# Kernel optimization log

Measured on AMD Instinct MI355X. Metric: run time of the kernel, lower is better.

## Reference

```python
import jax, jax.numpy as jnp
import numpy as np

N, H, E, A, T = 50000, 128, 800000, 16, 4


def setup_inputs() -> dict:
    key = jax.random.key(0)
    ks = jax.random.split(key, 12)
    s = 1.0 / np.sqrt(H + A)
    s2 = 1.0 / np.sqrt(H)
    return {
        "h": jax.random.normal(ks[0], (N, H), dtype=jnp.float32),
        "edge_index": jax.random.randint(ks[1], (2, E), 0, N, dtype=jnp.int32),
        "edge_type": jax.random.randint(ks[2], (E,), 0, T, dtype=jnp.int32),
        "edge_attr": jax.random.normal(ks[3], (E, A), dtype=jnp.float32),
        # per-edge-type 2-layer MLP params
        "W1": jax.random.uniform(ks[4], (T, H + A, H), minval=-s, maxval=s, dtype=jnp.float32),
        "b1": jax.random.uniform(ks[5], (T, H), minval=-s, maxval=s, dtype=jnp.float32),
        "W2": jax.random.uniform(ks[6], (T, H, H), minval=-s2, maxval=s2, dtype=jnp.float32),
        "b2": jax.random.uniform(ks[7], (T, H), minval=-s2, maxval=s2, dtype=jnp.float32),
        # GRUCell params (torch layout: [3H, H] with gate order r, z, n)
        "w_ih": jax.random.uniform(ks[8], (3 * H, H), minval=-s2, maxval=s2, dtype=jnp.float32),
        "w_hh": jax.random.uniform(ks[9], (3 * H, H), minval=-s2, maxval=s2, dtype=jnp.float32),
        "b_ih": jax.random.uniform(ks[10], (3 * H,), minval=-s2, maxval=s2, dtype=jnp.float32),
        "b_hh": jax.random.uniform(ks[11], (3 * H,), minval=-s2, maxval=s2, dtype=jnp.float32),
    }


def reference(h, edge_index, edge_type, edge_attr, W1, b1, W2, b2, w_ih, w_hh, b_ih, b_hh):
    src, dst = edge_index[0], edge_index[1]
    h_in = jnp.concatenate([h[src], edge_attr], axis=-1)  # [E, H+A]
    # per-edge-type MLP; loop over small fixed num_edge_types, mask-select
    m = jnp.zeros((h_in.shape[0], H), dtype=h.dtype)
    for t in range(T):
        mt = jax.nn.relu(h_in @ W1[t] + b1[t]) @ W2[t] + b2[t]  # [E, H]
        m = jnp.where((edge_type == t)[:, None], mt, m)
    # scatter-add messages to destination nodes
    msg = jax.ops.segment_sum(m, dst, num_segments=h.shape[0])  # [N, H]
    # GRUCell(msg, h) with torch gate order r, z, n
    gi = msg @ w_ih.T + b_ih  # [N, 3H]
    gh = h @ w_hh.T + b_hh
    i_r, i_z, i_n = jnp.split(gi, 3, axis=-1)
    h_r, h_z, h_n = jnp.split(gh, 3, axis=-1)
    r = jax.nn.sigmoid(i_r + h_r)
    z = jax.nn.sigmoid(i_z + h_z)
    n = jnp.tanh(i_n + r * h_n)
    return (1.0 - z) * n + z * h
```

## Files before the change

kernel.cpp:

```cpp
#include <hip/hip_runtime.h>
#include <stdint.h>

#define Hh 128
#define Aa 16
#define Tt 4
#define K1 144
#define K1P 160
#define W1T_LD 168
#define WG_LD  136

typedef float f32x4 __attribute__((ext_vector_type(4)));
typedef __bf16 bf16x8 __attribute__((ext_vector_type(8)));
typedef unsigned short u16x8 __attribute__((ext_vector_type(8)));
typedef unsigned short u16x4 __attribute__((ext_vector_type(4)));
typedef unsigned short u16x2 __attribute__((ext_vector_type(2)));

static __device__ __forceinline__ unsigned short f2bf(float f) {
    unsigned u = __builtin_bit_cast(unsigned, f);
    u += 0x7fffu + ((u >> 16) & 1u);
    return (unsigned short)(u >> 16);
}

static __device__ __forceinline__ float bf2f(unsigned short u) {
    return __builtin_bit_cast(float, (unsigned)u << 16);
}

static __device__ __forceinline__ bf16x8 pack8(const float* __restrict__ x) {
    f32x4 a = *(const f32x4*)x;
    f32x4 b = *(const f32x4*)(x + 4);
    u16x8 t;
    t[0] = f2bf(a[0]); t[1] = f2bf(a[1]); t[2] = f2bf(a[2]); t[3] = f2bf(a[3]);
    t[4] = f2bf(b[0]); t[5] = f2bf(b[1]); t[6] = f2bf(b[2]); t[7] = f2bf(b[3]);
    return __builtin_bit_cast(bf16x8, t);
}

static __device__ __forceinline__ bf16x8 zero_bf8() {
    u16x8 z = {0, 0, 0, 0, 0, 0, 0, 0};
    return __builtin_bit_cast(bf16x8, z);
}

__global__ void cast_all_kernel(
    const float* __restrict__ h, const float* __restrict__ wih, const float* __restrict__ whh,
    unsigned short* __restrict__ h_bf, unsigned short* __restrict__ wihb,
    unsigned short* __restrict__ whhb, int n0, int n1, int n2)
{
    int i = blockIdx.x * blockDim.x + threadIdx.x;
    if (i >= n2) return;
    const float* s; unsigned short* d; int off;
    if (i < n0)      { s = h;   d = h_bf; off = i; }
    else if (i < n1) { s = wih; d = wihb; off = i - n0; }
    else             { s = whh; d = whhb; off = i - n1; }
    f32x4 v = *(const f32x4*)(s + (size_t)off * 4);
    u16x4 o;
    o[0] = f2bf(v[0]); o[1] = f2bf(v[1]); o[2] = f2bf(v[2]); o[3] = f2bf(v[3]);
    *(u16x4*)(d + (size_t)off * 4) = o;
}

__global__ void w1t_kernel(const float* __restrict__ W1, unsigned short* __restrict__ W1Tbf) {
    __shared__ float tile[16][129];
    const int b = blockIdx.x;
    const int t = b / 10, kb = b % 10;
    const int k0 = kb * 16;
    const int tid = threadIdx.x;
    for (int e = tid; e < 16 * 128; e += 256) {
        int k = e >> 7, n = e & 127;
        tile[k][n] = (k0 + k < K1) ? W1[((size_t)t * K1 + k0 + k) * Hh + n] : 0.f;
    }
    __syncthreads();
    for (int e = tid; e < 128 * 16; e += 256) {
        int n = e >> 4, kk = e & 15;
        W1Tbf[((size_t)t * Hh + n) * K1P + k0 + kk] = f2bf(tile[kk][n]);
    }
}

__global__ void w2t_kernel(const float* __restrict__ W2, unsigned short* __restrict__ W2Tbf) {
    __shared__ float tile[16][129];
    const int b = blockIdx.x;
    const int t = b >> 3, kb = b & 7;
    const int k0 = kb * 16;
    const int tid = threadIdx.x;
    for (int e = tid; e < 16 * 128; e += 256) {
        int k = e >> 7, n = e & 127;
        tile[k][n] = W2[((size_t)t * Hh + k0 + k) * Hh + n];
    }
    __syncthreads();
    for (int e = tid; e < 128 * 16; e += 256) {
        int n = e >> 4, kk = e & 15;
        W2Tbf[((size_t)t * Hh + n) * Hh + k0 + kk] = f2bf(tile[kk][n]);
    }
}

__global__ void hist_kernel(const int* __restrict__ et, const int* __restrict__ eidx,
                            int E, int N, int* __restrict__ cnt, unsigned* __restrict__ rank) {
    for (int i = blockIdx.x * blockDim.x + threadIdx.x; i < E; i += gridDim.x * blockDim.x) {
        int tt = et[i];
        unsigned rD = (unsigned)atomicAdd(&cnt[tt * N + eidx[E + i]], 1);
        unsigned rS = (unsigned)atomicAdd(&cnt[4 * N + tt * N + eidx[i]], 1);
        rank[i] = rD | (rS << 16);
    }
}

__global__ void scanA_kernel(const int* __restrict__ deg2, int nb, int* __restrict__ bsum) {
    __shared__ int red[256];
    const int t = threadIdx.x;
    const int i0 = blockIdx.x * 1024 + t * 4;
    int s = 0;
    #pragma unroll
    for (int j = 0; j < 4; j++) if (i0 + j < nb) s += deg2[i0 + j];
    red[t] = s; __syncthreads();
    for (int d = 128; d > 0; d >>= 1) {
        if (t < d) red[t] += red[t + d];
        __syncthreads();
    }
    if (t == 0) bsum[blockIdx.x] = red[0];
}

__global__ void scanB_kernel(int* __restrict__ bsum, int nblocks,
                             int* __restrict__ rowptrD, int fourN, int E) {
    __shared__ int ts[512];
    const int t = threadIdx.x;
    int v = (t < nblocks) ? bsum[t] : 0;
    ts[t] = v; __syncthreads();
    for (int d = 1; d < 512; d <<= 1) {
        int x = (t >= d) ? ts[t - d] : 0;
        __syncthreads();
        ts[t] += x;
        __syncthreads();
    }
    if (t < nblocks) bsum[t] = ts[t] - v;
    if (t == 0) rowptrD[fourN] = E;
}

__global__ void scanC_kernel(int* __restrict__ cur, int nb, int fourN,
                             const int* __restrict__ bsum, int* __restrict__ rowptrD) {
    __shared__ int ts[256];
    const int t = threadIdx.x;
    const int i0 = blockIdx.x * 1024 + t * 4;
    int v[4];
    #pragma unroll
    for (int j = 0; j < 4; j++) v[j] = (i0 + j < nb) ? cur[i0 + j] : 0;
    int s = v[0] + v[1] + v[2] + v[3];
    ts[t] = s; __syncthreads();
    for (int d = 1; d < 256; d <<= 1) {
        int x = (t >= d) ? ts[t - d] : 0;
        __syncthreads();
        ts[t] += x;
        __syncthreads();
    }
    int run = bsum[blockIdx.x] + ts[t] - s;
    #pragma unroll
    for (int j = 0; j < 4; j++) {
        if (i0 + j < nb) {
            if (i0 + j < fourN) rowptrD[i0 + j] = run;
            cur[i0 + j] = run;
            run += v[j];
        }
    }
}

__global__ void fill2_kernel(const int* __restrict__ et, const int* __restrict__ eidx,
                             int E, int N, const int* __restrict__ binstart,
                             const unsigned* __restrict__ rank, int4* __restrict__ rec) {
    for (int i = blockIdx.x * blockDim.x + threadIdx.x; i < E; i += gridDim.x * blockDim.x) {
        int tt = et[i];
        int d = eidx[E + i], s = eidx[i];
        unsigned r = rank[i];
        int posD = binstart[tt * N + d] + (int)(r & 0xffffu);
        int posS = binstart[4 * N + tt * N + s] + (int)(r >> 16) - E;
        rec[posS] = make_int4(s, i, posD, 0);
    }
}

__global__ __launch_bounds__(512) void l1_kernel(
    const unsigned short* __restrict__ h_bf, const int4* __restrict__ rec,
    const float* __restrict__ eattr, const unsigned short* __restrict__ W1Tbf,
    const float* __restrict__ b1, const int* __restrict__ rowptrD,
    unsigned short* __restrict__ Yg, int N)
{
    __shared__ unsigned short W1T[128 * W1T_LD];
    __shared__ float b1s[128];
    const int t = blockIdx.x & 3;
    const int lb = blockIdx.x >> 2;
    const int nbk = gridDim.x >> 2;
    const int tid = threadIdx.x;

    for (int idx = tid; idx < (Hh * K1P) / 8; idx += 512) {
        int n = idx / 20, c = (idx % 20) * 8;
        *(u16x8*)&W1T[n * W1T_LD + c] =
            *(const u16x8*)&W1Tbf[((size_t)t * Hh + n) * K1P + c];
    }
    if (tid < 128) b1s[tid] = b1[t * Hh + tid];
    __syncthreads();

    const int tstart = rowptrD[t * N];
    const int tend = rowptrD[(t + 1) * N];
    const int cnt = tend - tstart;
    const int ntiles = (cnt + 255) >> 8;
    const int w = tid >> 6, lane = tid & 63;
    const int l15 = lane & 15, q = lane >> 4;
    const int tl = tend - 1;

    for (int tile = lb; tile < ntiles; tile += nbk) {
        const int p0 = tstart + tile * 256 + w * 32;
        const bool va = p0 + l15 < tend, vb = p0 + 16 + l15 < tend;
        const int4 ra = rec[min(p0 + l15, tl)];
        const int4 rb = rec[min(p0 + 16 + l15, tl)];
        const unsigned short* __restrict__ hA = h_bf + (size_t)ra.x * Hh;
        const unsigned short* __restrict__ hB = h_bf + (size_t)rb.x * Hh;

        f32x4 acc[8][2];
        #pragma unroll
        for (int mt = 0; mt < 8; mt++) {
            acc[mt][0] = (f32x4){0.f, 0.f, 0.f, 0.f};
            acc[mt][1] = (f32x4){0.f, 0.f, 0.f, 0.f};
        }

        #pragma unroll
        for (int ks = 0; ks < 5; ks++) {
            const int k0 = ks * 32;
            bf16x8 fb_a, fb_b;
            if (ks < 4) {
                fb_a = __builtin_bit_cast(bf16x8, *(const u16x8*)(hA + k0 + q * 8));
                fb_b = __builtin_bit_cast(bf16x8, *(const u16x8*)(hB + k0 + q * 8));
            } else if (q < 2) {
                fb_a = pack8(eattr + (size_t)ra.y * Aa + q * 8);
                fb_b = pack8(eattr + (size_t)rb.y * Aa + q * 8);
            } else {
                fb_a = zero_bf8();
                fb_b = zero_bf8();
            }
            #pragma unroll
            for (int mt = 0; mt < 8; mt++) {
                bf16x8 fa = *(const bf16x8*)&W1T[(mt * 16 + l15) * W1T_LD + k0 + q * 8];
                acc[mt][0] = __builtin_amdgcn_mfma_f32_16x16x32_bf16(fa, fb_a, acc[mt][0], 0, 0, 0);
                acc[mt][1] = __builtin_amdgcn_mfma_f32_16x16x32_bf16(fa, fb_b, acc[mt][1], 0, 0, 0);
            }
        }

        #pragma unroll
        for (int g = 0; g < 2; g++) {
            if (g ? vb : va) {
                const int yp = g ? rb.z : ra.z;
                unsigned short* __restrict__ o = Yg + (size_t)yp * Hh + q * 4;
                #pragma unroll
                for (int mt = 0; mt < 8; mt++) {
                    f32x4 bias = *(const f32x4*)&b1s[mt * 16 + q * 4];
                    u16x4 y;
                    #pragma unroll
                    for (int i = 0; i < 4; i++) {
                        float v = acc[mt][g][i] + bias[i];
                        y[i] = f2bf(v > 0.f ? v : 0.f);
                    }
                    *(u16x4*)(o + mt * 16) = y;
                }
            }
        }
    }
}

__global__ __launch_bounds__(256) void sumY_kernel(
    unsigned short* __restrict__ Yg, const int* __restrict__ rowptrD, int fourN)
{
    const int gid = blockIdx.x * blockDim.x + threadIdx.x;
    const int stride = gridDim.x * blockDim.x;
    const int total = fourN * 4;
    for (int task = gid; task < total; task += stride) {
        const int p = task >> 2;
        const int q = task & 3;
        const int seg = rowptrD[p];
        const int len = rowptrD[p + 1] - seg;
        if (len <= 1) continue;
        float asum[32];
        #pragma unroll
        for (int i = 0; i < 32; i++) asum[i] = 0.f;
        for (int j = 0; j < len; j++) {
            const unsigned short* __restrict__ yr = Yg + (size_t)(seg + j) * Hh;
            #pragma unroll
            for (int ks = 0; ks < 4; ks++) {
                u16x8 yv = *(const u16x8*)(yr + ks * 32 + q * 8);
                #pragma unroll
                for (int e = 0; e < 8; e++) asum[ks * 8 + e] += bf2f(yv[e]);
            }
        }
        unsigned short* __restrict__ wr = Yg + (size_t)seg * Hh;
        #pragma unroll
        for (int ks = 0; ks < 4; ks++) {
            u16x8 o;
            #pragma unroll
            for (int e = 0; e < 8; e++) o[e] = f2bf(asum[ks * 8 + e]);
            *(u16x8*)(wr + ks * 32 + q * 8) = o;
        }
    }
}

__global__ __launch_bounds__(256) void gemm2_kernel(
    const unsigned short* __restrict__ Yg, const int* __restrict__ rowptrD,
    const unsigned short* __restrict__ W2Tbf, const float* __restrict__ b2,
    unsigned short* __restrict__ msgb, int N)
{
    __shared__ unsigned short W2T[128 * WG_LD];
    __shared__ float b2s[512];
    __shared__ int cntS[4 * 64];
    const int tid = threadIdx.x;
    const int w = tid >> 6, lane = tid & 63;
    const int l15 = lane & 15, q = lane >> 4;
    const int nodebase = blockIdx.x * 64 + w * 16;
    const int nA = min(nodebase + l15, N - 1);

    b2s[tid] = b2[tid];
    b2s[tid + 256] = b2[tid + 256];

    f32x4 acc[8];
    #pragma unroll
    for (int ct = 0; ct < 8; ct++) acc[ct] = (f32x4){0.f, 0.f, 0.f, 0.f};

    for (int t = 0; t < Tt; t++) {
        __syncthreads();
        for (int idx = tid; idx < (Hh * Hh) / 8; idx += 256) {
            int n = idx >> 4, c = (idx & 15) * 8;
            *(u16x8*)&W2T[n * WG_LD + c] =
                *(const u16x8*)&W2Tbf[((size_t)t * Hh + n) * Hh + c];
        }
        __syncthreads();

        const int seg = rowptrD[(size_t)t * N + nA];
        const int len = rowptrD[(size_t)t * N + nA + 1] - seg;
        cntS[w * 64 + t * 16 + l15] = len;

        bf16x8 fa[4];
        if (len > 0) {
            const unsigned short* __restrict__ yr = Yg + (size_t)seg * Hh;
            #pragma unroll
            for (int ks = 0; ks < 4; ks++)
                fa[ks] = __builtin_bit_cast(bf16x8, *(const u16x8*)(yr + ks * 32 + q * 8));
        } else {
            #pragma unroll
            for (int ks = 0; ks < 4; ks++) fa[ks] = zero_bf8();
        }

        #pragma unroll
        for (int ks = 0; ks < 4; ks++) {
            #pragma unroll
            for (int ct = 0; ct < 8; ct++) {
                bf16x8 fb = *(const bf16x8*)&W2T[(ct * 16 + l15) * WG_LD + ks * 32 + q * 8];
                acc[ct] = __builtin_amdgcn_mfma_f32_16x16x32_bf16(fa[ks], fb, acc[ct], 0, 0, 0);
            }
        }
    }
    __syncthreads();

    #pragma unroll
    for (int ct = 0; ct < 8; ct++) {
        const int c = ct * 16 + l15;
        #pragma unroll
        for (int i = 0; i < 4; i++) {
            int node = nodebase + q * 4 + i;
            if (node < N) {
                float bias = 0.f;
                #pragma unroll
                for (int t = 0; t < Tt; t++)
                    bias += (float)cntS[w * 64 + t * 16 + q * 4 + i] * b2s[t * 128 + c];
                msgb[(size_t)node * Hh + c] = f2bf(acc[ct][i] + bias);
            }
        }
    }
}

__global__ __launch_bounds__(512) void gru_kernel(
    const float* __restrict__ h, const unsigned short* __restrict__ h_bf,
    const unsigned short* __restrict__ msgb,
    const unsigned short* __restrict__ wihb, const unsigned short* __restrict__ whhb,
    const float* __restrict__ b_ih, const float* __restrict__ b_hh,
    float* __restrict__ out, int N)
{
    __shared__ unsigned short Wg[128 * WG_LD];
    const int tid = threadIdx.x;
    const int lane = tid & 63;
    const int l15 = lane & 15, q = lane >> 4;
    const int w = tid >> 6;
    const int nodebase = blockIdx.x * 128 + w * 16;
    const int nA = min(nodebase + l15, N - 1);

    bf16x8 fm[4], fh[4];
    #pragma unroll
    for (int ks = 0; ks < 4; ks++) {
        fm[ks] = __builtin_bit_cast(bf16x8, *(const u16x8*)(msgb + (size_t)nA * Hh + ks * 32 + q * 8));
        fh[ks] = __builtin_bit_cast(bf16x8, *(const u16x8*)(h_bf + (size_t)nA * Hh + ks * 32 + q * 8));
    }

    u16x8 pre[4];
    const int so = tid >> 4, sk = (tid & 15) * 8;
    auto loadg = [&](const unsigned short* __restrict__ Ws, int gate) {
        #pragma unroll
        for (int i = 0; i < 4; i++)
            pre[i] = *(const u16x8*)&Ws[(size_t)gate * Hh * Hh + (size_t)(so + i * 32) * Hh + sk];
    };
    auto commit = [&]() {
        __syncthreads();
        #pragma unroll
        for (int i = 0; i < 4; i++)
            *(u16x8*)&Wg[(so + i * 32) * WG_LD + sk] = pre[i];
        __syncthreads();
    };
    auto matmul = [&](f32x4* acc, const bf16x8* fa) {
        #pragma unroll
        for (int ks = 0; ks < 4; ks++) {
            #pragma unroll
            for (int ct = 0; ct < 8; ct++) {
                bf16x8 fb = *(const bf16x8*)&Wg[(ct * 16 + l15) * WG_LD + ks * 32 + q * 8];
                acc[ct] = __builtin_amdgcn_mfma_f32_16x16x32_bf16(fa[ks], fb, acc[ct], 0, 0, 0);
            }
        }
    };

    f32x4 gr[8], gin[8], ghn[8];
    #pragma unroll
    for (int ct = 0; ct < 8; ct++) {
        gr[ct] = (f32x4){0.f, 0.f, 0.f, 0.f};
        gin[ct] = (f32x4){0.f, 0.f, 0.f, 0.f};
        ghn[ct] = (f32x4){0.f, 0.f, 0.f, 0.f};
    }

    loadg(wihb, 0);
    commit(); loadg(whhb, 0); matmul(gr, fm);
    commit(); loadg(wihb, 2); matmul(gr, fh);
    commit(); loadg(whhb, 2); matmul(gin, fm);
    commit(); loadg(wihb, 1); matmul(ghn, fh);

    #pragma unroll
    for (int ct = 0; ct < 8; ct++) {
        const int c = ct * 16 + l15;
        float bir = b_ih[c], bhr = b_hh[c];
        float bin = b_ih[256 + c], bhn = b_hh[256 + c];
        #pragma unroll
        for (int i = 0; i < 4; i++) {
            float rv = 1.f / (1.f + __expf(-(gr[ct][i] + bir + bhr)));
            gin[ct][i] = gin[ct][i] + bin + rv * (ghn[ct][i] + bhn);
        }
    }
    #pragma unroll
    for (int ct = 0; ct < 8; ct++) gr[ct] = (f32x4){0.f, 0.f, 0.f, 0.f};

    commit(); loadg(whhb, 1); matmul(gr, fm);
    commit();                 matmul(gr, fh);

    #pragma unroll
    for (int ct = 0; ct < 8; ct++) {
        const int c = ct * 16 + l15;
        float biz = b_ih[128 + c], bhz = b_hh[128 + c];
        #pragma unroll
        for (int i = 0; i < 4; i++) {
            int node = nodebase + q * 4 + i;
            if (node < N) {
                float zv = 1.f / (1.f + __expf(-(gr[ct][i] + biz + bhz)));
                float e2 = __expf(-2.f * gin[ct][i]);
                float nv = (1.f - e2) / (1.f + e2);
                float hv = h[(size_t)node * Hh + c];
                out[(size_t)node * Hh + c] = (1.f - zv) * nv + zv * hv;
            }
        }
    }
}

static inline size_t align256(size_t x) { return (x + 255) & ~(size_t)255; }

extern "C" void kernel_launch(void* const* d_in, const int* in_sizes, int n_in,
                              void* d_out, int out_size, void* d_ws, size_t ws_size,
                              hipStream_t stream)
{
    const float* h     = (const float*)d_in[0];
    const int*   eidx  = (const int*)d_in[1];
    const int*   et    = (const int*)d_in[2];
    const float* eattr = (const float*)d_in[3];
    const float* W1    = (const float*)d_in[4];
    const float* b1    = (const float*)d_in[5];
    const float* W2    = (const float*)d_in[6];
    const float* b2    = (const float*)d_in[7];
    const float* w_ih  = (const float*)d_in[8];
    const float* w_hh  = (const float*)d_in[9];
    const float* b_ih  = (const float*)d_in[10];
    const float* b_hh  = (const float*)d_in[11];

    const int N = in_sizes[0] / Hh;
    const int E = in_sizes[1] / 2;
    const int nb = 8 * N;
    const int sblocks = (nb + 1023) / 1024;

    char* p = (char*)d_ws;
    unsigned short* msgb = (unsigned short*)p; p += align256((size_t)N * Hh * sizeof(unsigned short));
    unsigned short* Yg = (unsigned short*)p;   p += align256((size_t)E * Hh * sizeof(unsigned short));
    int4* rec = (int4*)p;               p += align256((size_t)E * sizeof(int4));
    unsigned* rank = (unsigned*)p;      p += align256((size_t)E * sizeof(unsigned));
    int* rowptrD = (int*)p;             p += align256(((size_t)4 * N + 1) * sizeof(int));
    int* cur = (int*)p;                 p += align256((size_t)nb * sizeof(int));
    int* bsum = (int*)p;                p += align256(1024 * sizeof(int));
    unsigned short* h_bf = (unsigned short*)p; p += align256((size_t)N * Hh * sizeof(unsigned short));
    unsigned short* W1Tbf = (unsigned short*)p; p += align256((size_t)Tt * Hh * K1P * sizeof(unsigned short));
    unsigned short* W2Tbf = (unsigned short*)p; p += align256((size_t)Tt * Hh * Hh * sizeof(unsigned short));
    unsigned short* wihb = (unsigned short*)p; p += align256((size_t)3 * Hh * Hh * sizeof(unsigned short));
    unsigned short* whhb = (unsigned short*)p; p += align256((size_t)3 * Hh * Hh * sizeof(unsigned short));

    hipMemsetAsync(cur, 0, (size_t)nb * sizeof(int), stream);

    {
        int n4h = N * Hh / 4, n4g = 3 * Hh * Hh / 4;
        int c0 = n4h, c1 = c0 + n4g, c2 = c1 + n4g;
        cast_all_kernel<<<(c2 + 255) / 256, 256, 0, stream>>>(
            h, w_ih, w_hh, h_bf, wihb, whhb, c0, c1, c2);
    }
    w1t_kernel<<<Tt * 10, 256, 0, stream>>>(W1, W1Tbf);
    w2t_kernel<<<Tt * 8, 256, 0, stream>>>(W2, W2Tbf);

    hist_kernel<<<1024, 256, 0, stream>>>(et, eidx, E, N, cur, rank);
    scanA_kernel<<<sblocks, 256, 0, stream>>>(cur, nb, bsum);
    scanB_kernel<<<1, 512, 0, stream>>>(bsum, sblocks, rowptrD, 4 * N, E);
    scanC_kernel<<<sblocks, 256, 0, stream>>>(cur, nb, 4 * N, bsum, rowptrD);
    fill2_kernel<<<1024, 256, 0, stream>>>(et, eidx, E, N, cur, rank, rec);

    l1_kernel<<<2048, 512, 0, stream>>>(h_bf, rec, eattr, W1Tbf, b1, rowptrD, Yg, N);
    sumY_kernel<<<2048, 256, 0, stream>>>(Yg, rowptrD, 4 * N);
    gemm2_kernel<<<(N + 63) / 64, 256, 0, stream>>>(Yg, rowptrD, W2Tbf, b2, msgb, N);

    int gblocks = (N + 127) / 128;
    gru_kernel<<<gblocks, 512, 0, stream>>>(h, h_bf, msgb, wihb, whhb, b_ih, b_hh, (float*)d_out, N);
}
```

Baseline: 528.8 us.

## Drop source-sorted edge ordering, fuse segment sum into second GEMM, read weights from global

Edges are now sorted only by (type, destination), removing the second histogram atomic and the source-ordered record array; records shrink to int2 and layer-1 writes go straight to the sorted position. The separate sumY pass is folded into the second GEMM kernel, which accumulates each segment's rows in fp32 before the MFMA. Both GEMM kernels stop staging weights in LDS and load the bf16 weight fragments directly from global/L2, and the l1 grid is halved. The trade is less locality on h gathers (no source ordering), heavier per-thread segment loops in the GEMM, and weight fragment reads from global instead of LDS.

```diff
diff --git a/kernel.cpp b/kernel.cpp
--- a/kernel.cpp
+++ b/kernel.cpp
@@ -6,14 +6,12 @@
 #define Tt 4
 #define K1 144
 #define K1P 160
-#define W1T_LD 168
 #define WG_LD  136
 
 typedef float f32x4 __attribute__((ext_vector_type(4)));
 typedef __bf16 bf16x8 __attribute__((ext_vector_type(8)));
 typedef unsigned short u16x8 __attribute__((ext_vector_type(8)));
 typedef unsigned short u16x4 __attribute__((ext_vector_type(4)));
-typedef unsigned short u16x2 __attribute__((ext_vector_type(2)));
 
 static __device__ __forceinline__ unsigned short f2bf(float f) {
     unsigned u = __builtin_bit_cast(unsigned, f);
@@ -93,10 +91,7 @@
 __global__ void hist_kernel(const int* __restrict__ et, const int* __restrict__ eidx,
                             int E, int N, int* __restrict__ cnt, unsigned* __restrict__ rank) {
     for (int i = blockIdx.x * blockDim.x + threadIdx.x; i < E; i += gridDim.x * blockDim.x) {
-        int tt = et[i];
-        unsigned rD = (unsigned)atomicAdd(&cnt[tt * N + eidx[E + i]], 1);
-        unsigned rS = (unsigned)atomicAdd(&cnt[4 * N + tt * N + eidx[i]], 1);
-        rank[i] = rD | (rS << 16);
+        rank[i] = (unsigned)atomicAdd(&cnt[et[i] * N + eidx[E + i]], 1);
     }
 }
 
@@ -131,7 +126,7 @@
     if (t == 0) rowptrD[fourN] = E;
 }
 
-__global__ void scanC_kernel(int* __restrict__ cur, int nb, int fourN,
+__global__ void scanC_kernel(int* __restrict__ cur, int nb,
                              const int* __restrict__ bsum, int* __restrict__ rowptrD) {
     __shared__ int ts[256];
     const int t = threadIdx.x;
@@ -151,7 +146,7 @@
     #pragma unroll
     for (int j = 0; j < 4; j++) {
         if (i0 + j < nb) {
-            if (i0 + j < fourN) rowptrD[i0 + j] = run;
+            rowptrD[i0 + j] = run;
             cur[i0 + j] = run;
             run += v[j];
         }
@@ -160,35 +155,24 @@
 
 __global__ void fill2_kernel(const int* __restrict__ et, const int* __restrict__ eidx,
                              int E, int N, const int* __restrict__ binstart,
-                             const unsigned* __restrict__ rank, int4* __restrict__ rec) {
+                             const unsigned* __restrict__ rank, int2* __restrict__ rec) {
     for (int i = blockIdx.x * blockDim.x + threadIdx.x; i < E; i += gridDim.x * blockDim.x) {
-        int tt = et[i];
-        int d = eidx[E + i], s = eidx[i];
-        unsigned r = rank[i];
-        int posD = binstart[tt * N + d] + (int)(r & 0xffffu);
-        int posS = binstart[4 * N + tt * N + s] + (int)(r >> 16) - E;
-        rec[posS] = make_int4(s, i, posD, 0);
+        int posD = binstart[et[i] * N + eidx[E + i]] + (int)rank[i];
+        rec[posD] = make_int2(eidx[i], i);
     }
 }
 
 __global__ __launch_bounds__(512) void l1_kernel(
-    const unsigned short* __restrict__ h_bf, const int4* __restrict__ rec,
+    const unsigned short* __restrict__ h_bf, const int2* __restrict__ rec,
     const float* __restrict__ eattr, const unsigned short* __restrict__ W1Tbf,
     const float* __restrict__ b1, const int* __restrict__ rowptrD,
     unsigned short* __restrict__ Yg, int N)
 {
-    __shared__ unsigned short W1T[128 * W1T_LD];
     __shared__ float b1s[128];
     const int t = blockIdx.x & 3;
     const int lb = blockIdx.x >> 2;
     const int nbk = gridDim.x >> 2;
     const int tid = threadIdx.x;
-
-    for (int idx = tid; idx < (Hh * K1P) / 8; idx += 512) {
-        int n = idx / 20, c = (idx % 20) * 8;
-        *(u16x8*)&W1T[n * W1T_LD + c] =
-            *(const u16x8*)&W1Tbf[((size_t)t * Hh + n) * K1P + c];
-    }
     if (tid < 128) b1s[tid] = b1[t * Hh + tid];
     __syncthreads();
 
@@ -199,12 +183,16 @@
     const int w = tid >> 6, lane = tid & 63;
     const int l15 = lane & 15, q = lane >> 4;
     const int tl = tend - 1;
+    const unsigned short* __restrict__ Wt =
+        W1Tbf + (size_t)t * Hh * K1P + (size_t)l15 * K1P + q * 8;
 
     for (int tile = lb; tile < ntiles; tile += nbk) {
+        __builtin_amdgcn_sched_barrier(0);
         const int p0 = tstart + tile * 256 + w * 32;
-        const bool va = p0 + l15 < tend, vb = p0 + 16 + l15 < tend;
-        const int4 ra = rec[min(p0 + l15, tl)];
-        const int4 rb = rec[min(p0 + 16 + l15, tl)];
+        const int pa = p0 + l15, pb = p0 + 16 + l15;
+        const bool va = pa < tend, vb = pb < tend;
+        const int2 ra = rec[min(pa, tl)];
+        const int2 rb = rec[min(pb, tl)];
         const unsigned short* __restrict__ hA = h_bf + (size_t)ra.x * Hh;
         const unsigned short* __restrict__ hB = h_bf + (size_t)rb.x * Hh;
 
@@ -215,14 +203,21 @@
             acc[mt][1] = (f32x4){0.f, 0.f, 0.f, 0.f};
         }
 
-        #pragma unroll
-        for (int ks = 0; ks < 5; ks++) {
+        #pragma unroll 1
+        for (int ks = 0; ks < 4; ks++) {
             const int k0 = ks * 32;
+            bf16x8 fb_a = __builtin_bit_cast(bf16x8, *(const u16x8*)(hA + k0 + q * 8));
+            bf16x8 fb_b = __builtin_bit_cast(bf16x8, *(const u16x8*)(hB + k0 + q * 8));
+            #pragma unroll
+            for (int mt = 0; mt < 8; mt++) {
+                bf16x8 fa = *(const bf16x8*)(Wt + (size_t)mt * 16 * K1P + k0);
+                acc[mt][0] = __builtin_amdgcn_mfma_f32_16x16x32_bf16(fa, fb_a, acc[mt][0], 0, 0, 0);
+                acc[mt][1] = __builtin_amdgcn_mfma_f32_16x16x32_bf16(fa, fb_b, acc[mt][1], 0, 0, 0);
+            }
+        }
+        {
             bf16x8 fb_a, fb_b;
-            if (ks < 4) {
-                fb_a = __builtin_bit_cast(bf16x8, *(const u16x8*)(hA + k0 + q * 8));
-                fb_b = __builtin_bit_cast(bf16x8, *(const u16x8*)(hB + k0 + q * 8));
-            } else if (q < 2) {
+            if (q < 2) {
                 fb_a = pack8(eattr + (size_t)ra.y * Aa + q * 8);
                 fb_b = pack8(eattr + (size_t)rb.y * Aa + q * 8);
             } else {
@@ -231,17 +226,17 @@
             }
             #pragma unroll
             for (int mt = 0; mt < 8; mt++) {
-                bf16x8 fa = *(const bf16x8*)&W1T[(mt * 16 + l15) * W1T_LD + k0 + q * 8];
+                bf16x8 fa = *(const bf16x8*)(Wt + (size_t)mt * 16 * K1P + 128);
                 acc[mt][0] = __builtin_amdgcn_mfma_f32_16x16x32_bf16(fa, fb_a, acc[mt][0], 0, 0, 0);
                 acc[mt][1] = __builtin_amdgcn_mfma_f32_16x16x32_bf16(fa, fb_b, acc[mt][1], 0, 0, 0);
             }
         }
+        __builtin_amdgcn_sched_barrier(0);
 
         #pragma unroll
         for (int g = 0; g < 2; g++) {
             if (g ? vb : va) {
-                const int yp = g ? rb.z : ra.z;
-                unsigned short* __restrict__ o = Yg + (size_t)yp * Hh + q * 4;
+                unsigned short* __restrict__ o = Yg + (size_t)(g ? pb : pa) * Hh + q * 4;
                 #pragma unroll
                 for (int mt = 0; mt < 8; mt++) {
                     f32x4 bias = *(const f32x4*)&b1s[mt * 16 + q * 4];
@@ -255,50 +250,15 @@
                 }
             }
         }
-    }
-}
-
-__global__ __launch_bounds__(256) void sumY_kernel(
-    unsigned short* __restrict__ Yg, const int* __restrict__ rowptrD, int fourN)
-{
-    const int gid = blockIdx.x * blockDim.x + threadIdx.x;
-    const int stride = gridDim.x * blockDim.x;
-    const int total = fourN * 4;
-    for (int task = gid; task < total; task += stride) {
-        const int p = task >> 2;
-        const int q = task & 3;
-        const int seg = rowptrD[p];
-        const int len = rowptrD[p + 1] - seg;
-        if (len <= 1) continue;
-        float asum[32];
-        #pragma unroll
-        for (int i = 0; i < 32; i++) asum[i] = 0.f;
-        for (int j = 0; j < len; j++) {
-            const unsigned short* __restrict__ yr = Yg + (size_t)(seg + j) * Hh;
-            #pragma unroll
-            for (int ks = 0; ks < 4; ks++) {
-                u16x8 yv = *(const u16x8*)(yr + ks * 32 + q * 8);
-                #pragma unroll
-                for (int e = 0; e < 8; e++) asum[ks * 8 + e] += bf2f(yv[e]);
-            }
-        }
-        unsigned short* __restrict__ wr = Yg + (size_t)seg * Hh;
-        #pragma unroll
-        for (int ks = 0; ks < 4; ks++) {
-            u16x8 o;
-            #pragma unroll
-            for (int e = 0; e < 8; e++) o[e] = f2bf(asum[ks * 8 + e]);
-            *(u16x8*)(wr + ks * 32 + q * 8) = o;
-        }
-    }
-}
-
-__global__ __launch_bounds__(256) void gemm2_kernel(
+        __builtin_amdgcn_sched_barrier(0);
+    }
+}
+
+__global__ __launch_bounds__(256) void zgemm_kernel(
     const unsigned short* __restrict__ Yg, const int* __restrict__ rowptrD,
     const unsigned short* __restrict__ W2Tbf, const float* __restrict__ b2,
     unsigned short* __restrict__ msgb, int N)
 {
-    __shared__ unsigned short W2T[128 * WG_LD];
     __shared__ float b2s[512];
     __shared__ int cntS[4 * 64];
     const int tid = threadIdx.x;
@@ -309,41 +269,41 @@
 
     b2s[tid] = b2[tid];
     b2s[tid + 256] = b2[tid + 256];
+    const unsigned short* __restrict__ W2l =
+        W2Tbf + (size_t)l15 * Hh + q * 8;
 
     f32x4 acc[8];
     #pragma unroll
     for (int ct = 0; ct < 8; ct++) acc[ct] = (f32x4){0.f, 0.f, 0.f, 0.f};
 
     for (int t = 0; t < Tt; t++) {
-        __syncthreads();
-        for (int idx = tid; idx < (Hh * Hh) / 8; idx += 256) {
-            int n = idx >> 4, c = (idx & 15) * 8;
-            *(u16x8*)&W2T[n * WG_LD + c] =
-                *(const u16x8*)&W2Tbf[((size_t)t * Hh + n) * Hh + c];
-        }
-        __syncthreads();
-
         const int seg = rowptrD[(size_t)t * N + nA];
         const int len = rowptrD[(size_t)t * N + nA + 1] - seg;
         cntS[w * 64 + t * 16 + l15] = len;
 
-        bf16x8 fa[4];
-        if (len > 0) {
-            const unsigned short* __restrict__ yr = Yg + (size_t)seg * Hh;
-            #pragma unroll
-            for (int ks = 0; ks < 4; ks++)
-                fa[ks] = __builtin_bit_cast(bf16x8, *(const u16x8*)(yr + ks * 32 + q * 8));
-        } else {
-            #pragma unroll
-            for (int ks = 0; ks < 4; ks++) fa[ks] = zero_bf8();
+        float asum[32];
+        #pragma unroll
+        for (int i = 0; i < 32; i++) asum[i] = 0.f;
+        for (int j = 0; j < len; j++) {
+            const unsigned short* __restrict__ yr = Yg + (size_t)(seg + j) * Hh;
+            #pragma unroll
+            for (int ks = 0; ks < 4; ks++) {
+                u16x8 yv = *(const u16x8*)(yr + ks * 32 + q * 8);
+                #pragma unroll
+                for (int e = 0; e < 8; e++) asum[ks * 8 + e] += bf2f(yv[e]);
+            }
         }
 
         #pragma unroll
         for (int ks = 0; ks < 4; ks++) {
+            u16x8 fr;
+            #pragma unroll
+            for (int e = 0; e < 8; e++) fr[e] = f2bf(asum[ks * 8 + e]);
+            bf16x8 fa = __builtin_bit_cast(bf16x8, fr);
             #pragma unroll
             for (int ct = 0; ct < 8; ct++) {
-                bf16x8 fb = *(const bf16x8*)&W2T[(ct * 16 + l15) * WG_LD + ks * 32 + q * 8];
-                acc[ct] = __builtin_amdgcn_mfma_f32_16x16x32_bf16(fa[ks], fb, acc[ct], 0, 0, 0);
+                bf16x8 fb = *(const bf16x8*)(W2l + ((size_t)t * Hh + ct * 16) * Hh + ks * 32);
+                acc[ct] = __builtin_amdgcn_mfma_f32_16x16x32_bf16(fa, fb, acc[ct], 0, 0, 0);
             }
         }
     }
@@ -483,13 +443,13 @@
 
     const int N = in_sizes[0] / Hh;
     const int E = in_sizes[1] / 2;
-    const int nb = 8 * N;
+    const int nb = 4 * N;
     const int sblocks = (nb + 1023) / 1024;
 
     char* p = (char*)d_ws;
     unsigned short* msgb = (unsigned short*)p; p += align256((size_t)N * Hh * sizeof(unsigned short));
     unsigned short* Yg = (unsigned short*)p;   p += align256((size_t)E * Hh * sizeof(unsigned short));
-    int4* rec = (int4*)p;               p += align256((size_t)E * sizeof(int4));
+    int2* rec = (int2*)p;               p += align256((size_t)E * sizeof(int2));
     unsigned* rank = (unsigned*)p;      p += align256((size_t)E * sizeof(unsigned));
     int* rowptrD = (int*)p;             p += align256(((size_t)4 * N + 1) * sizeof(int));
     int* cur = (int*)p;                 p += align256((size_t)nb * sizeof(int));
@@ -514,12 +474,11 @@
     hist_kernel<<<1024, 256, 0, stream>>>(et, eidx, E, N, cur, rank);
     scanA_kernel<<<sblocks, 256, 0, stream>>>(cur, nb, bsum);
     scanB_kernel<<<1, 512, 0, stream>>>(bsum, sblocks, rowptrD, 4 * N, E);
-    scanC_kernel<<<sblocks, 256, 0, stream>>>(cur, nb, 4 * N, bsum, rowptrD);
+    scanC_kernel<<<sblocks, 256, 0, stream>>>(cur, nb, bsum, rowptrD);
     fill2_kernel<<<1024, 256, 0, stream>>>(et, eidx, E, N, cur, rank, rec);
 
-    l1_kernel<<<2048, 512, 0, stream>>>(h_bf, rec, eattr, W1Tbf, b1, rowptrD, Yg, N);
-    sumY_kernel<<<2048, 256, 0, stream>>>(Yg, rowptrD, 4 * N);
-    gemm2_kernel<<<(N + 63) / 64, 256, 0, stream>>>(Yg, rowptrD, W2Tbf, b2, msgb, N);
+    l1_kernel<<<1024, 512, 0, stream>>>(h_bf, rec, eattr, W1Tbf, b1, rowptrD, Yg, N);
+    zgemm_kernel<<<(N + 63) / 64, 256, 0, stream>>>(Yg, rowptrD, W2Tbf, b2, msgb, N);
 
     int gblocks = (N + 127) / 128;
     gru_kernel<<<gblocks, 512, 0, stream>>>(h, h_bf, msgb, wihb, whhb, b_ih, b_hh, (float*)d_out, N);
```

Result: no change. 536.3 us (+1.4%).
